# Kernel optimization log

Hardware: AMD Instinct MI355X
Metric: run time of the kernel (lower is better)

The kernel has to match this reference:

```python
import jax, jax.numpy as jnp
import numpy as np

LN_EPS = 1e-5


def _gather(x, idx):
    # x: [B, N, C], idx: [B, N, K] -> [B, N, K, C]
    return jax.vmap(lambda xb, ib: xb[ib])(x, idx)


def setup_inputs() -> dict:
    key = jax.random.key(0)
    ks = jax.random.split(key, 8)
    B, N, K, C_in, C_out, GEO = 2, 16384, 32, 128, 128, 10
    return {
        "points": jax.random.normal(ks[0], (B, N, 3), dtype=jnp.float32),
        "features": jax.random.normal(ks[1], (B, N, C_in), dtype=jnp.float32),
        "grouped_idx": jax.random.randint(ks[2], (B, N, K), 0, N, dtype=jnp.int32),
        "w_pos": jax.random.normal(ks[3], (GEO, C_in), dtype=jnp.float32) * (GEO ** -0.5),
        "b_pos": jnp.zeros((C_in,), jnp.float32),
        "w_gcm": jax.random.normal(ks[4], (C_in, C_in), dtype=jnp.float32) * (C_in ** -0.5),
        "b_gcm": jnp.zeros((C_in,), jnp.float32),
        "w_out": jax.random.normal(ks[5], (C_in, C_out), dtype=jnp.float32) * (C_in ** -0.5),
        "b_out": jnp.zeros((C_out,), jnp.float32),
        "ln_g": jnp.ones((C_out,), jnp.float32),
        "ln_b": jnp.zeros((C_out,), jnp.float32),
    }


def reference(points, features, grouped_idx, w_pos, b_pos, w_gcm, b_gcm,
              w_out, b_out, ln_g, ln_b):
    # gather neighbor coords and features: [B, N, K, *]
    grouped_pts = _gather(points, grouped_idx)
    xyz = points[..., 0:3]                      # [B, N, 3]
    grouped_xyz = grouped_pts[..., 0:3]         # [B, N, K, 3]
    center = xyz[:, :, None, :]                 # [B, N, 1, 3]
    diff = grouped_xyz - center                 # xi - xj
    dist = jnp.linalg.norm(diff, axis=-1, keepdims=True)  # ||xi - xj||
    K = grouped_xyz.shape[2]
    geo = jnp.concatenate(
        [jnp.broadcast_to(center, grouped_xyz.shape), grouped_xyz, diff, dist],
        axis=-1)                                # [B, N, K, 10]
    expanded_f = geo @ w_pos + b_pos            # pos_proj -> [B, N, K, C_in]
    grouped_f = _gather(features, grouped_idx)  # [B, N, K, C_in]
    h = jax.nn.relu((grouped_f + expanded_f) @ w_gcm + b_gcm)  # gcm_layer
    pooled = jnp.max(h, axis=2)                 # maxpooling over neighbors
    res = pooled + features                     # residual
    o = res @ w_out + b_out                     # out Linear
    mu = jnp.mean(o, axis=-1, keepdims=True)
    var = jnp.mean((o - mu) ** 2, axis=-1, keepdims=True)
    o = (o - mu) * jax.lax.rsqrt(var + LN_EPS) * ln_g + ln_b  # LayerNorm
    return jax.nn.relu(o)
```

## Files before the change

kernel.cpp:

```cpp
#include <hip/hip_runtime.h>
#include <hip/hip_bf16.h>
#include <math.h>

typedef __attribute__((ext_vector_type(8))) short short8;
typedef __attribute__((ext_vector_type(4))) float float4v;
typedef unsigned short ushort_t;

constexpr int NPTS = 32768;
constexpr int NN   = 16384;
constexpr int KK   = 32;
constexpr int CC   = 128;
constexpr int GRP  = 16;
constexpr int SG   = 40;
constexpr int SR   = 136;
#define LN_EPS 1e-5f

constexpr size_t WS_WP   = 0;
constexpr size_t WS_WO   = 40960;
constexpr size_t WS_BE   = 73728;
constexpr size_t WS_FB   = 74240;
constexpr size_t WS_NEED = WS_FB + (size_t)NPTS * CC * 2;

__device__ __forceinline__ short f2bs(float x) {
    return (short)__builtin_bit_cast(unsigned short, __float2bfloat16(x));
}
__device__ __forceinline__ float bs2f(ushort_t u) {
    return __uint_as_float(((unsigned)u) << 16);
}

__global__ __launch_bounds__(256) void prep_kernel(
    const float* __restrict__ features,
    const float* __restrict__ w_pos, const float* __restrict__ b_pos,
    const float* __restrict__ w_gcm, const float* __restrict__ b_gcm,
    const float* __restrict__ w_out,
    short* __restrict__ wsWp, short* __restrict__ wsWo, float* __restrict__ wsBeff,
    ushort_t* __restrict__ featbf)
{
    const int t = threadIdx.x;
    const int blk = blockIdx.x;

    if (blk >= 2) {
        const size_t base = (size_t)(blk - 2) * 2048 + (size_t)t * 8;
        const float4* fp = (const float4*)(features + base);
        const float4 a = fp[0], b = fp[1];
        short8 v;
        v[0]=f2bs(a.x); v[1]=f2bs(a.y); v[2]=f2bs(a.z); v[3]=f2bs(a.w);
        v[4]=f2bs(b.x); v[5]=f2bs(b.y); v[6]=f2bs(b.z); v[7]=f2bs(b.w);
        *(short8*)(featbf + base) = v;
        return;
    }
    if (blk == 1) {
        for (int e = t; e < 128 * 128; e += 256) {
            int j = e & 7, n = (e >> 3) & 127, g = e >> 10;
            wsWo[e] = f2bs(w_out[(g * 8 + j) * 128 + n]);
        }
        return;
    }
    __shared__ float sW[128 * 128];
    __shared__ float sPG[10 * 128];
    for (int e = t; e < 4096; e += 256) ((float4*)sW)[e] = ((const float4*)w_gcm)[e];
    __syncthreads();
    {
        const int c  = t & 127;
        const int gb = t >> 7;
        for (int gi = 0; gi < 5; ++gi) {
            const int g = gi * 2 + gb;
            float s = 0.f;
            for (int r = 0; r < 128; ++r) s += w_pos[g * 128 + r] * sW[r * 128 + c];
            sPG[g * 128 + c] = s;
        }
        if (t < 128) {
            float wb = b_gcm[t];
            for (int r = 0; r < 128; ++r) wb += b_pos[r] * sW[r * 128 + t];
            wsBeff[t] = wb;
        }
    }
    __syncthreads();
    for (int e = t; e < 20 * 128 * 8; e += 256) {
        const int j = e & 7, n = (e >> 3) & 127, g = e >> 10;
        const int k = g * 8 + j;
        const float v = (k < 128) ? sW[k * 128 + n] : (k < 138 ? sPG[(k - 128) * 128 + n] : 0.f);
        wsWp[e] = f2bs(v);
    }
}

template<int DMA>
__global__ __launch_bounds__(256) void bridge_main(
    const float* __restrict__ points, const float* __restrict__ features,
    const int*   __restrict__ gidx,
    const short* __restrict__ wsWp, const short* __restrict__ wsWo,
    const float* __restrict__ wsBeff, const ushort_t* __restrict__ featbf,
    const float* __restrict__ b_out, const float* __restrict__ ln_g,
    const float* __restrict__ ln_b,
    float* __restrict__ out)
{
    __shared__ short sA[2][KK * CC];
    __shared__ short sG[2][KK * SG];
    __shared__ short sRes[GRP * SR];
    __shared__ int   sIdx[GRP * KK];
    __shared__ float sPS[4][GRP], sPQ[4][GRP];

    const int t = threadIdx.x, wv = t >> 6, lane = t & 63;
    const int quad = (t >> 4) & 3, m = t & 15;
    const int g0 = blockIdx.x * GRP;
    const int nbase = (g0 >= NN) ? NN : 0;
    const int col0 = wv * 32 + m;

    sIdx[t]       = gidx[(size_t)g0 * KK + t];
    sIdx[t + 256] = gidx[(size_t)g0 * KK + t + 256];
    if (t < 128) {
        const int b = t >> 6, r = (t >> 1) & 31, h = t & 1;
        *(short8*)&sG[b][r * SG + 16 + h * 8] = (short8)0;
    }

    short8 bWp[5][2];
    #pragma unroll
    for (int ks = 0; ks < 5; ++ks)
        #pragma unroll
        for (int ntl = 0; ntl < 2; ++ntl)
            bWp[ks][ntl] = *((const short8*)wsWp + ((ks * 4 + quad) * 128 + col0 + ntl * 16));
    float beffv[2] = { wsBeff[col0], wsBeff[col0 + 16] };

    __syncthreads();

    const int r0 = wv * 4 + (lane >> 4);
    const int pc = lane & 15;
    const int gc = pc ^ r0;

    float4 ff0a, ff0b, ff1a, ff1b;
    float gcx, gcy, gcz, ggx, ggy, ggz;

    auto issue_dma = [&](int p, int buf) {
        const int kn0 = nbase + sIdx[p * KK + r0];
        const int kn1 = nbase + sIdx[p * KK + r0 + 16];
        const ushort_t* gp0 = featbf + (size_t)kn0 * CC + gc * 8;
        const ushort_t* gp1 = featbf + (size_t)kn1 * CC + gc * 8;
        short* l0 = &sA[buf][(wv * 4) * CC];
        short* l1 = &sA[buf][(wv * 4 + 16) * CC];
        __builtin_amdgcn_global_load_lds((const __attribute__((address_space(1))) void*)gp0,
                                         (__attribute__((address_space(3))) void*)l0, 16, 0, 0);
        __builtin_amdgcn_global_load_lds((const __attribute__((address_space(1))) void*)gp1,
                                         (__attribute__((address_space(3))) void*)l1, 16, 0, 0);
    };
    auto fb_load = [&](int p) {
        const int kn0 = nbase + sIdx[p * KK + r0];
        const int kn1 = nbase + sIdx[p * KK + r0 + 16];
        const float4* f0 = (const float4*)(features + (size_t)kn0 * CC + gc * 8);
        const float4* f1 = (const float4*)(features + (size_t)kn1 * CC + gc * 8);
        ff0a = f0[0]; ff0b = f0[1]; ff1a = f1[0]; ff1b = f1[1];
    };
    auto fb_store = [&](int buf) {
        short8 v;
        v[0]=f2bs(ff0a.x); v[1]=f2bs(ff0a.y); v[2]=f2bs(ff0a.z); v[3]=f2bs(ff0a.w);
        v[4]=f2bs(ff0b.x); v[5]=f2bs(ff0b.y); v[6]=f2bs(ff0b.z); v[7]=f2bs(ff0b.w);
        *(short8*)&sA[buf][r0 * CC + pc * 8] = v;
        v[0]=f2bs(ff1a.x); v[1]=f2bs(ff1a.y); v[2]=f2bs(ff1a.z); v[3]=f2bs(ff1a.w);
        v[4]=f2bs(ff1b.x); v[5]=f2bs(ff1b.y); v[6]=f2bs(ff1b.z); v[7]=f2bs(ff1b.w);
        *(short8*)&sA[buf][(r0 + 16) * CC + pc * 8] = v;
    };
    auto geo_load = [&](int p) {
        if (lane < 8) {
            const int j  = wv * 8 + lane;
            const int pt = g0 + p;
            const int kn = nbase + sIdx[p * KK + j];
            gcx = points[(size_t)pt * 3 + 0]; gcy = points[(size_t)pt * 3 + 1]; gcz = points[(size_t)pt * 3 + 2];
            ggx = points[(size_t)kn * 3 + 0]; ggy = points[(size_t)kn * 3 + 1]; ggz = points[(size_t)kn * 3 + 2];
        }
    };
    auto geo_store = [&](int buf) {
        if (lane < 8) {
            const int j = wv * 8 + lane;
            const float dx = ggx - gcx, dy = ggy - gcy, dz = ggz - gcz;
            const float dist = sqrtf(dx * dx + dy * dy + dz * dz);
            short8 v0, v1 = (short8)0;
            v0[0]=f2bs(gcx); v0[1]=f2bs(gcy); v0[2]=f2bs(gcz);
            v0[3]=f2bs(ggx); v0[4]=f2bs(ggy); v0[5]=f2bs(ggz);
            v0[6]=f2bs(dx);  v0[7]=f2bs(dy);
            v1[0]=f2bs(dz);  v1[1]=f2bs(dist);
            *(short8*)&sG[buf][j * SG + 0] = v0;
            *(short8*)&sG[buf][j * SG + 8] = v1;
        }
    };

    if constexpr (DMA) issue_dma(0, 0); else fb_load(0);
    geo_load(0);
    if constexpr (!DMA) fb_store(0);
    geo_store(0);
    __syncthreads();

    int offA[4];
    #pragma unroll
    for (int ks = 0; ks < 4; ++ks) offA[ks] = m * CC + (((ks * 4 + quad) ^ m) * 8);
    const int offG = m * SG + quad * 8;

    for (int p = 0; p < GRP; ++p) {
        const int buf = p & 1, nbuf = buf ^ 1;
        if (p + 1 < GRP) {
            if constexpr (DMA) issue_dma(p + 1, nbuf); else fb_load(p + 1);
            geo_load(p + 1);
        }

        const short* ab = sA[buf];
        const short* ag = sG[buf];
        float4v acc[2][2] = {};
        #pragma unroll
        for (int ks = 0; ks < 4; ++ks) {
            const short8 a0 = *(const short8*)(ab + offA[ks]);
            const short8 a1 = *(const short8*)(ab + offA[ks] + 16 * CC);
            acc[0][0] = __builtin_amdgcn_mfma_f32_16x16x32_bf16(a0, bWp[ks][0], acc[0][0], 0, 0, 0);
            acc[0][1] = __builtin_amdgcn_mfma_f32_16x16x32_bf16(a0, bWp[ks][1], acc[0][1], 0, 0, 0);
            acc[1][0] = __builtin_amdgcn_mfma_f32_16x16x32_bf16(a1, bWp[ks][0], acc[1][0], 0, 0, 0);
            acc[1][1] = __builtin_amdgcn_mfma_f32_16x16x32_bf16(a1, bWp[ks][1], acc[1][1], 0, 0, 0);
        }
        {
            const short8 a0 = *(const short8*)(ag + offG);
            const short8 a1 = *(const short8*)(ag + offG + 16 * SG);
            acc[0][0] = __builtin_amdgcn_mfma_f32_16x16x32_bf16(a0, bWp[4][0], acc[0][0], 0, 0, 0);
            acc[0][1] = __builtin_amdgcn_mfma_f32_16x16x32_bf16(a0, bWp[4][1], acc[0][1], 0, 0, 0);
            acc[1][0] = __builtin_amdgcn_mfma_f32_16x16x32_bf16(a1, bWp[4][0], acc[1][0], 0, 0, 0);
            acc[1][1] = __builtin_amdgcn_mfma_f32_16x16x32_bf16(a1, bWp[4][1], acc[1][1], 0, 0, 0);
        }

        if (p + 1 < GRP) {
            if constexpr (!DMA) fb_store(nbuf);
            geo_store(nbuf);
        }

        const int pt = g0 + p;
        #pragma unroll
        for (int ntl = 0; ntl < 2; ++ntl) {
            float v = acc[0][ntl][0];
            #pragma unroll
            for (int r = 1; r < 4; ++r) v = fmaxf(v, acc[0][ntl][r]);
            #pragma unroll
            for (int r = 0; r < 4; ++r) v = fmaxf(v, acc[1][ntl][r]);
            v = fmaxf(v, __shfl_xor(v, 16));
            v = fmaxf(v, __shfl_xor(v, 32));
            v = fmaxf(v + beffv[ntl], 0.f);
            float fc;
            if constexpr (DMA) fc = bs2f(featbf[(size_t)pt * CC + col0 + ntl * 16]);
            else               fc = features[(size_t)pt * CC + col0 + ntl * 16];
            const float res = v + fc;
            if (quad == 0) sRes[p * SR + col0 + ntl * 16] = f2bs(res);
        }
        __syncthreads();
    }

    short8 bWo[4][2];
    #pragma unroll
    for (int ks = 0; ks < 4; ++ks)
        #pragma unroll
        for (int ntl = 0; ntl < 2; ++ntl)
            bWo[ks][ntl] = *((const short8*)wsWo + ((ks * 4 + quad) * 128 + col0 + ntl * 16));

    const short* rm = sRes + m * SR;
    float4v acc2[2] = {};
    #pragma unroll
    for (int ks = 0; ks < 4; ++ks) {
        const short8 a = *(const short8*)(rm + ks * 32 + quad * 8);
        acc2[0] = __builtin_amdgcn_mfma_f32_16x16x32_bf16(a, bWo[ks][0], acc2[0], 0, 0, 0);
        acc2[1] = __builtin_amdgcn_mfma_f32_16x16x32_bf16(a, bWo[ks][1], acc2[1], 0, 0, 0);
    }

    const float boutv[2] = { b_out[col0], b_out[col0 + 16] };
    const float lngv[2]  = { ln_g[col0], ln_g[col0 + 16] };
    const float lnbv[2]  = { ln_b[col0], ln_b[col0 + 16] };

    #pragma unroll
    for (int r = 0; r < 4; ++r) {
        const float o0 = acc2[0][r] + boutv[0];
        const float o1 = acc2[1][r] + boutv[1];
        float ss = o0 + o1, qq = o0 * o0 + o1 * o1;
        #pragma unroll
        for (int d = 1; d < 16; d <<= 1) { ss += __shfl_xor(ss, d); qq += __shfl_xor(qq, d); }
        if (m == 0) { sPS[wv][quad * 4 + r] = ss; sPQ[wv][quad * 4 + r] = qq; }
    }
    __syncthreads();

    #pragma unroll
    for (int r = 0; r < 4; ++r) {
        const int R = quad * 4 + r;
        const float S = sPS[0][R] + sPS[1][R] + sPS[2][R] + sPS[3][R];
        const float Q = sPQ[0][R] + sPQ[1][R] + sPQ[2][R] + sPQ[3][R];
        const float mu  = S * (1.f / 128.f);
        const float var = fmaxf(Q * (1.f / 128.f) - mu * mu, 0.f);
        const float rstd = rsqrtf(var + LN_EPS);
        const float o0 = acc2[0][r] + boutv[0];
        const float o1 = acc2[1][r] + boutv[1];
        const size_t base = (size_t)(g0 + R) * CC;
        out[base + col0]      = fmaxf((o0 - mu) * rstd * lngv[0] + lnbv[0], 0.f);
        out[base + col0 + 16] = fmaxf((o1 - mu) * rstd * lngv[1] + lnbv[1], 0.f);
    }
}

extern "C" void kernel_launch(void* const* d_in, const int* in_sizes, int n_in,
                              void* d_out, int out_size, void* d_ws, size_t ws_size,
                              hipStream_t stream) {
    const float* points   = (const float*)d_in[0];
    const float* features = (const float*)d_in[1];
    const int*   gidx     = (const int*)  d_in[2];
    const float* w_pos    = (const float*)d_in[3];
    const float* b_pos    = (const float*)d_in[4];
    const float* w_gcm    = (const float*)d_in[5];
    const float* b_gcm    = (const float*)d_in[6];
    const float* w_out    = (const float*)d_in[7];
    const float* b_out    = (const float*)d_in[8];
    const float* ln_g     = (const float*)d_in[9];
    const float* ln_b     = (const float*)d_in[10];
    float* out = (float*)d_out;

    char* ws = (char*)d_ws;
    short*    wsWp   = (short*)(ws + WS_WP);
    short*    wsWo   = (short*)(ws + WS_WO);
    float*    wsBeff = (float*)(ws + WS_BE);
    ushort_t* featbf = (ushort_t*)(ws + WS_FB);

    const bool use_dma = (ws_size >= WS_NEED);
    const int prep_blocks = use_dma ? (2 + NPTS * CC / 2048) : 2;

    hipLaunchKernelGGL(prep_kernel, dim3(prep_blocks), dim3(256), 0, stream,
                       features, w_pos, b_pos, w_gcm, b_gcm, w_out,
                       wsWp, wsWo, wsBeff, featbf);
    if (use_dma) {
        hipLaunchKernelGGL((bridge_main<1>), dim3(NPTS / GRP), dim3(256), 0, stream,
                           points, features, gidx, wsWp, wsWo, wsBeff, featbf,
                           b_out, ln_g, ln_b, out);
    } else {
        hipLaunchKernelGGL((bridge_main<0>), dim3(NPTS / GRP), dim3(256), 0, stream,
                           points, features, gidx, wsWp, wsWo, wsBeff, featbf,
                           b_out, ln_g, ln_b, out);
    }
}
```

Before: 174.9 us.

## Process two points per iteration with waves split by point and channel half

The main loop now handles a pair of points per iteration. Each pair of waves owns one point, and each wave covers 64 output channels (4 column tiles) instead of 32. This halves the loop trips and barriers, doubles the MFMA work per A-fragment load, and prefetches the residual features a stage early. The single prep kernel is split into a two-block weight-prep kernel and a separate feature-conversion kernel, and the w_out transpose is staged through shared memory. In exchange the doubled shared buffers and larger per-thread weight fragments raise register and LDS pressure, which may lower occupancy, and the LayerNorm stores are now done by only half the waves.

```diff
diff --git a/kernel.cpp b/kernel.cpp
--- a/kernel.cpp
+++ b/kernel.cpp
@@ -3,6 +3,7 @@
 #include <math.h>
 
 typedef __attribute__((ext_vector_type(8))) short short8;
+typedef __attribute__((ext_vector_type(4))) short short4v;
 typedef __attribute__((ext_vector_type(4))) float float4v;
 typedef unsigned short ushort_t;
 
@@ -28,36 +29,25 @@
     return __uint_as_float(((unsigned)u) << 16);
 }
 
-__global__ __launch_bounds__(256) void prep_kernel(
-    const float* __restrict__ features,
+__global__ __launch_bounds__(256) void prep_weights(
     const float* __restrict__ w_pos, const float* __restrict__ b_pos,
     const float* __restrict__ w_gcm, const float* __restrict__ b_gcm,
     const float* __restrict__ w_out,
-    short* __restrict__ wsWp, short* __restrict__ wsWo, float* __restrict__ wsBeff,
-    ushort_t* __restrict__ featbf)
+    short* __restrict__ wsWp, short* __restrict__ wsWo, float* __restrict__ wsBeff)
 {
+    __shared__ float sW[128 * 128];
+    __shared__ float sPG[10 * 128];
     const int t = threadIdx.x;
-    const int blk = blockIdx.x;
-
-    if (blk >= 2) {
-        const size_t base = (size_t)(blk - 2) * 2048 + (size_t)t * 8;
-        const float4* fp = (const float4*)(features + base);
-        const float4 a = fp[0], b = fp[1];
-        short8 v;
-        v[0]=f2bs(a.x); v[1]=f2bs(a.y); v[2]=f2bs(a.z); v[3]=f2bs(a.w);
-        v[4]=f2bs(b.x); v[5]=f2bs(b.y); v[6]=f2bs(b.z); v[7]=f2bs(b.w);
-        *(short8*)(featbf + base) = v;
-        return;
-    }
-    if (blk == 1) {
+
+    if (blockIdx.x == 1) {
+        for (int e = t; e < 4096; e += 256) ((float4*)sW)[e] = ((const float4*)w_out)[e];
+        __syncthreads();
         for (int e = t; e < 128 * 128; e += 256) {
             int j = e & 7, n = (e >> 3) & 127, g = e >> 10;
-            wsWo[e] = f2bs(w_out[(g * 8 + j) * 128 + n]);
+            wsWo[e] = f2bs(sW[(g * 8 + j) * 128 + n]);
         }
         return;
     }
-    __shared__ float sW[128 * 128];
-    __shared__ float sPG[10 * 128];
     for (int e = t; e < 4096; e += 256) ((float4*)sW)[e] = ((const float4*)w_gcm)[e];
     __syncthreads();
     {
@@ -81,6 +71,19 @@
         const int k = g * 8 + j;
         const float v = (k < 128) ? sW[k * 128 + n] : (k < 138 ? sPG[(k - 128) * 128 + n] : 0.f);
         wsWp[e] = f2bs(v);
+    }
+}
+
+__global__ __launch_bounds__(256) void prep_convert(
+    const float* __restrict__ features, ushort_t* __restrict__ featbf)
+{
+    const int t = threadIdx.x;
+    #pragma unroll
+    for (int i = 0; i < 8; ++i) {
+        const int f4 = blockIdx.x * 2048 + i * 256 + t;
+        const float4 a = ((const float4*)features)[f4];
+        short4v v; v[0]=f2bs(a.x); v[1]=f2bs(a.y); v[2]=f2bs(a.z); v[3]=f2bs(a.w);
+        ((short4v*)featbf)[f4] = v;
     }
 }
 
@@ -94,82 +97,56 @@
     const float* __restrict__ ln_b,
     float* __restrict__ out)
 {
-    __shared__ short sA[2][KK * CC];
-    __shared__ short sG[2][KK * SG];
+    __shared__ short sA[2][2][KK * CC];
+    __shared__ short sG[2][2][KK * SG];
     __shared__ short sRes[GRP * SR];
     __shared__ int   sIdx[GRP * KK];
     __shared__ float sPS[4][GRP], sPQ[4][GRP];
 
     const int t = threadIdx.x, wv = t >> 6, lane = t & 63;
     const int quad = (t >> 4) & 3, m = t & 15;
+    const int ph = wv >> 1;
+    const int ch = wv & 1;
     const int g0 = blockIdx.x * GRP;
     const int nbase = (g0 >= NN) ? NN : 0;
-    const int col0 = wv * 32 + m;
 
     sIdx[t]       = gidx[(size_t)g0 * KK + t];
     sIdx[t + 256] = gidx[(size_t)g0 * KK + t + 256];
-    if (t < 128) {
-        const int b = t >> 6, r = (t >> 1) & 31, h = t & 1;
-        *(short8*)&sG[b][r * SG + 16 + h * 8] = (short8)0;
-    }
-
-    short8 bWp[5][2];
+    {
+        const int bu = t >> 7, te = (t >> 6) & 1, row = (t >> 1) & 31, h = t & 1;
+        *(short8*)&sG[bu][te][row * SG + 16 + h * 8] = (short8)0;
+    }
+
+    short8 bWp[5][4];
     #pragma unroll
     for (int ks = 0; ks < 5; ++ks)
         #pragma unroll
-        for (int ntl = 0; ntl < 2; ++ntl)
-            bWp[ks][ntl] = *((const short8*)wsWp + ((ks * 4 + quad) * 128 + col0 + ntl * 16));
-    float beffv[2] = { wsBeff[col0], wsBeff[col0 + 16] };
-
-    __syncthreads();
-
-    const int r0 = wv * 4 + (lane >> 4);
-    const int pc = lane & 15;
-    const int gc = pc ^ r0;
-
-    float4 ff0a, ff0b, ff1a, ff1b;
+        for (int n = 0; n < 4; ++n)
+            bWp[ks][n] = *((const short8*)wsWp + ((ks * 4 + quad) * 128 + ch * 64 + n * 16 + m));
+    float beffv[4];
+    #pragma unroll
+    for (int n = 0; n < 4; ++n) beffv[n] = wsBeff[ch * 64 + n * 16 + m];
+
+    __syncthreads();
+
     float gcx, gcy, gcz, ggx, ggy, ggz;
-
-    auto issue_dma = [&](int p, int buf) {
-        const int kn0 = nbase + sIdx[p * KK + r0];
-        const int kn1 = nbase + sIdx[p * KK + r0 + 16];
-        const ushort_t* gp0 = featbf + (size_t)kn0 * CC + gc * 8;
-        const ushort_t* gp1 = featbf + (size_t)kn1 * CC + gc * 8;
-        short* l0 = &sA[buf][(wv * 4) * CC];
-        short* l1 = &sA[buf][(wv * 4 + 16) * CC];
-        __builtin_amdgcn_global_load_lds((const __attribute__((address_space(1))) void*)gp0,
-                                         (__attribute__((address_space(3))) void*)l0, 16, 0, 0);
-        __builtin_amdgcn_global_load_lds((const __attribute__((address_space(1))) void*)gp1,
-                                         (__attribute__((address_space(3))) void*)l1, 16, 0, 0);
-    };
-    auto fb_load = [&](int p) {
-        const int kn0 = nbase + sIdx[p * KK + r0];
-        const int kn1 = nbase + sIdx[p * KK + r0 + 16];
-        const float4* f0 = (const float4*)(features + (size_t)kn0 * CC + gc * 8);
-        const float4* f1 = (const float4*)(features + (size_t)kn1 * CC + gc * 8);
-        ff0a = f0[0]; ff0b = f0[1]; ff1a = f1[0]; ff1b = f1[1];
-    };
-    auto fb_store = [&](int buf) {
-        short8 v;
-        v[0]=f2bs(ff0a.x); v[1]=f2bs(ff0a.y); v[2]=f2bs(ff0a.z); v[3]=f2bs(ff0a.w);
-        v[4]=f2bs(ff0b.x); v[5]=f2bs(ff0b.y); v[6]=f2bs(ff0b.z); v[7]=f2bs(ff0b.w);
-        *(short8*)&sA[buf][r0 * CC + pc * 8] = v;
-        v[0]=f2bs(ff1a.x); v[1]=f2bs(ff1a.y); v[2]=f2bs(ff1a.z); v[3]=f2bs(ff1a.w);
-        v[4]=f2bs(ff1b.x); v[5]=f2bs(ff1b.y); v[6]=f2bs(ff1b.z); v[7]=f2bs(ff1b.w);
-        *(short8*)&sA[buf][(r0 + 16) * CC + pc * 8] = v;
-    };
-    auto geo_load = [&](int p) {
-        if (lane < 8) {
-            const int j  = wv * 8 + lane;
-            const int pt = g0 + p;
-            const int kn = nbase + sIdx[p * KK + j];
+    float resn[4], resc[4];
+    float4 fb0[4], fb1[4];
+
+    auto geo_load = [&](int pair) {
+        if (lane < 16) {
+            const int e = wv * 16 + lane;
+            const int te = e >> 5, row = e & 31;
+            const int pt = g0 + pair * 2 + te;
+            const int kn = nbase + sIdx[(pair * 2 + te) * KK + row];
             gcx = points[(size_t)pt * 3 + 0]; gcy = points[(size_t)pt * 3 + 1]; gcz = points[(size_t)pt * 3 + 2];
             ggx = points[(size_t)kn * 3 + 0]; ggy = points[(size_t)kn * 3 + 1]; ggz = points[(size_t)kn * 3 + 2];
         }
     };
-    auto geo_store = [&](int buf) {
-        if (lane < 8) {
-            const int j = wv * 8 + lane;
+    auto geo_store = [&](int pair, int buf) {
+        if (lane < 16) {
+            const int e = wv * 16 + lane;
+            const int te = e >> 5, row = e & 31;
             const float dx = ggx - gcx, dy = ggy - gcy, dz = ggz - gcz;
             const float dist = sqrtf(dx * dx + dy * dy + dz * dz);
             short8 v0, v1 = (short8)0;
@@ -177,15 +154,57 @@
             v0[3]=f2bs(ggx); v0[4]=f2bs(ggy); v0[5]=f2bs(ggz);
             v0[6]=f2bs(dx);  v0[7]=f2bs(dy);
             v1[0]=f2bs(dz);  v1[1]=f2bs(dist);
-            *(short8*)&sG[buf][j * SG + 0] = v0;
-            *(short8*)&sG[buf][j * SG + 8] = v1;
-        }
-    };
-
-    if constexpr (DMA) issue_dma(0, 0); else fb_load(0);
+            *(short8*)&sG[buf][te][row * SG + 0] = v0;
+            *(short8*)&sG[buf][te][row * SG + 8] = v1;
+        }
+    };
+    auto res_load = [&](int pair) {
+        const int pt = g0 + pair * 2 + ph;
+        #pragma unroll
+        for (int n = 0; n < 4; ++n) {
+            if constexpr (DMA) resn[n] = bs2f(featbf[(size_t)pt * CC + ch * 64 + n * 16 + m]);
+            else               resn[n] = features[(size_t)pt * CC + ch * 64 + n * 16 + m];
+        }
+    };
+    auto gather_issue = [&](int pair, int buf) {
+        #pragma unroll
+        for (int i = 0; i < 4; ++i) {
+            const int e = wv * 4 + i;
+            const int te = e >> 3, rg = e & 7;
+            const int row = rg * 4 + (lane >> 4);
+            const int kn  = nbase + sIdx[(pair * 2 + te) * KK + row];
+            const int gc  = (lane & 15) ^ (row & 15);
+            if constexpr (DMA) {
+                const ushort_t* gp = featbf + (size_t)kn * CC + gc * 8;
+                short* lp = &sA[buf][te][rg * 4 * CC];
+                __builtin_amdgcn_global_load_lds((const __attribute__((address_space(1))) void*)gp,
+                                                 (__attribute__((address_space(3))) void*)lp, 16, 0, 0);
+            } else {
+                const float4* fp = (const float4*)(features + (size_t)kn * CC + gc * 8);
+                fb0[i] = fp[0]; fb1[i] = fp[1];
+            }
+        }
+    };
+    auto gather_store = [&](int buf) {
+        #pragma unroll
+        for (int i = 0; i < 4; ++i) {
+            const int e = wv * 4 + i;
+            const int te = e >> 3, rg = e & 7;
+            const int row = rg * 4 + (lane >> 4);
+            short8 v;
+            v[0]=f2bs(fb0[i].x); v[1]=f2bs(fb0[i].y); v[2]=f2bs(fb0[i].z); v[3]=f2bs(fb0[i].w);
+            v[4]=f2bs(fb1[i].x); v[5]=f2bs(fb1[i].y); v[6]=f2bs(fb1[i].z); v[7]=f2bs(fb1[i].w);
+            *(short8*)&sA[buf][te][row * CC + (lane & 15) * 8] = v;
+        }
+    };
+
     geo_load(0);
-    if constexpr (!DMA) fb_store(0);
-    geo_store(0);
+    res_load(0);
+    gather_issue(0, 0);
+    geo_store(0, 0);
+    if constexpr (!DMA) gather_store(0);
+    #pragma unroll
+    for (int n = 0; n < 4; ++n) resc[n] = resn[n];
     __syncthreads();
 
     int offA[4];
@@ -193,103 +212,115 @@
     for (int ks = 0; ks < 4; ++ks) offA[ks] = m * CC + (((ks * 4 + quad) ^ m) * 8);
     const int offG = m * SG + quad * 8;
 
-    for (int p = 0; p < GRP; ++p) {
-        const int buf = p & 1, nbuf = buf ^ 1;
-        if (p + 1 < GRP) {
-            if constexpr (DMA) issue_dma(p + 1, nbuf); else fb_load(p + 1);
-            geo_load(p + 1);
-        }
-
-        const short* ab = sA[buf];
-        const short* ag = sG[buf];
-        float4v acc[2][2] = {};
+    for (int pair = 0; pair < GRP / 2; ++pair) {
+        const int buf = pair & 1, nb = buf ^ 1;
+        if (pair < GRP / 2 - 1) {
+            geo_load(pair + 1);
+            res_load(pair + 1);
+            gather_issue(pair + 1, nb);
+        }
+
+        const short* at = sA[buf][ph];
+        const short* gt = sG[buf][ph];
+        float4v acc[2][4] = {};
         #pragma unroll
         for (int ks = 0; ks < 4; ++ks) {
-            const short8 a0 = *(const short8*)(ab + offA[ks]);
-            const short8 a1 = *(const short8*)(ab + offA[ks] + 16 * CC);
-            acc[0][0] = __builtin_amdgcn_mfma_f32_16x16x32_bf16(a0, bWp[ks][0], acc[0][0], 0, 0, 0);
-            acc[0][1] = __builtin_amdgcn_mfma_f32_16x16x32_bf16(a0, bWp[ks][1], acc[0][1], 0, 0, 0);
-            acc[1][0] = __builtin_amdgcn_mfma_f32_16x16x32_bf16(a1, bWp[ks][0], acc[1][0], 0, 0, 0);
-            acc[1][1] = __builtin_amdgcn_mfma_f32_16x16x32_bf16(a1, bWp[ks][1], acc[1][1], 0, 0, 0);
+            const short8 a0 = *(const short8*)(at + offA[ks]);
+            const short8 a1 = *(const short8*)(at + offA[ks] + 16 * CC);
+            #pragma unroll
+            for (int n = 0; n < 4; ++n) {
+                acc[0][n] = __builtin_amdgcn_mfma_f32_16x16x32_bf16(a0, bWp[ks][n], acc[0][n], 0, 0, 0);
+                acc[1][n] = __builtin_amdgcn_mfma_f32_16x16x32_bf16(a1, bWp[ks][n], acc[1][n], 0, 0, 0);
+            }
         }
         {
-            const short8 a0 = *(const short8*)(ag + offG);
-            const short8 a1 = *(const short8*)(ag + offG + 16 * SG);
-            acc[0][0] = __builtin_amdgcn_mfma_f32_16x16x32_bf16(a0, bWp[4][0], acc[0][0], 0, 0, 0);
-            acc[0][1] = __builtin_amdgcn_mfma_f32_16x16x32_bf16(a0, bWp[4][1], acc[0][1], 0, 0, 0);
-            acc[1][0] = __builtin_amdgcn_mfma_f32_16x16x32_bf16(a1, bWp[4][0], acc[1][0], 0, 0, 0);
-            acc[1][1] = __builtin_amdgcn_mfma_f32_16x16x32_bf16(a1, bWp[4][1], acc[1][1], 0, 0, 0);
-        }
-
-        if (p + 1 < GRP) {
-            if constexpr (!DMA) fb_store(nbuf);
-            geo_store(nbuf);
-        }
-
-        const int pt = g0 + p;
-        #pragma unroll
-        for (int ntl = 0; ntl < 2; ++ntl) {
-            float v = acc[0][ntl][0];
-            #pragma unroll
-            for (int r = 1; r < 4; ++r) v = fmaxf(v, acc[0][ntl][r]);
-            #pragma unroll
-            for (int r = 0; r < 4; ++r) v = fmaxf(v, acc[1][ntl][r]);
+            const short8 a0 = *(const short8*)(gt + offG);
+            const short8 a1 = *(const short8*)(gt + offG + 16 * SG);
+            #pragma unroll
+            for (int n = 0; n < 4; ++n) {
+                acc[0][n] = __builtin_amdgcn_mfma_f32_16x16x32_bf16(a0, bWp[4][n], acc[0][n], 0, 0, 0);
+                acc[1][n] = __builtin_amdgcn_mfma_f32_16x16x32_bf16(a1, bWp[4][n], acc[1][n], 0, 0, 0);
+            }
+        }
+
+        if (pair < GRP / 2 - 1) {
+            geo_store(pair + 1, nb);
+            if constexpr (!DMA) gather_store(nb);
+        }
+
+        const int prow = pair * 2 + ph;
+        #pragma unroll
+        for (int n = 0; n < 4; ++n) {
+            float v = acc[0][n][0];
+            #pragma unroll
+            for (int r = 1; r < 4; ++r) v = fmaxf(v, acc[0][n][r]);
+            #pragma unroll
+            for (int r = 0; r < 4; ++r) v = fmaxf(v, acc[1][n][r]);
             v = fmaxf(v, __shfl_xor(v, 16));
             v = fmaxf(v, __shfl_xor(v, 32));
-            v = fmaxf(v + beffv[ntl], 0.f);
-            float fc;
-            if constexpr (DMA) fc = bs2f(featbf[(size_t)pt * CC + col0 + ntl * 16]);
-            else               fc = features[(size_t)pt * CC + col0 + ntl * 16];
-            const float res = v + fc;
-            if (quad == 0) sRes[p * SR + col0 + ntl * 16] = f2bs(res);
-        }
+            v = fmaxf(v + beffv[n], 0.f);
+            const float res = v + resc[n];
+            if (quad == 0) sRes[prow * SR + ch * 64 + n * 16 + m] = f2bs(res);
+        }
+        #pragma unroll
+        for (int n = 0; n < 4; ++n) resc[n] = resn[n];
         __syncthreads();
     }
 
-    short8 bWo[4][2];
+    short8 bWo[4][4];
     #pragma unroll
     for (int ks = 0; ks < 4; ++ks)
         #pragma unroll
-        for (int ntl = 0; ntl < 2; ++ntl)
-            bWo[ks][ntl] = *((const short8*)wsWo + ((ks * 4 + quad) * 128 + col0 + ntl * 16));
+        for (int n = 0; n < 4; ++n)
+            bWo[ks][n] = *((const short8*)wsWo + ((ks * 4 + quad) * 128 + ch * 64 + n * 16 + m));
 
     const short* rm = sRes + m * SR;
-    float4v acc2[2] = {};
+    float4v acc2[4] = {};
     #pragma unroll
     for (int ks = 0; ks < 4; ++ks) {
-        const short8 a = *(const short8*)(rm + ks * 32 + quad * 8);
-        acc2[0] = __builtin_amdgcn_mfma_f32_16x16x32_bf16(a, bWo[ks][0], acc2[0], 0, 0, 0);
-        acc2[1] = __builtin_amdgcn_mfma_f32_16x16x32_bf16(a, bWo[ks][1], acc2[1], 0, 0, 0);
-    }
-
-    const float boutv[2] = { b_out[col0], b_out[col0 + 16] };
-    const float lngv[2]  = { ln_g[col0], ln_g[col0 + 16] };
-    const float lnbv[2]  = { ln_b[col0], ln_b[col0 + 16] };
+        const short8 a = *(const short8*)(rm + (ks * 4 + quad) * 8);
+        #pragma unroll
+        for (int n = 0; n < 4; ++n)
+            acc2[n] = __builtin_amdgcn_mfma_f32_16x16x32_bf16(a, bWo[ks][n], acc2[n], 0, 0, 0);
+    }
+
+    float boutv[4], lngv[4], lnbv[4];
+    #pragma unroll
+    for (int n = 0; n < 4; ++n) {
+        const int c = ch * 64 + n * 16 + m;
+        boutv[n] = b_out[c]; lngv[n] = ln_g[c]; lnbv[n] = ln_b[c];
+    }
 
     #pragma unroll
     for (int r = 0; r < 4; ++r) {
-        const float o0 = acc2[0][r] + boutv[0];
-        const float o1 = acc2[1][r] + boutv[1];
-        float ss = o0 + o1, qq = o0 * o0 + o1 * o1;
+        float ss = 0.f, qq = 0.f;
+        #pragma unroll
+        for (int n = 0; n < 4; ++n) {
+            const float o = acc2[n][r] + boutv[n];
+            ss += o; qq += o * o;
+        }
         #pragma unroll
         for (int d = 1; d < 16; d <<= 1) { ss += __shfl_xor(ss, d); qq += __shfl_xor(qq, d); }
         if (m == 0) { sPS[wv][quad * 4 + r] = ss; sPQ[wv][quad * 4 + r] = qq; }
     }
     __syncthreads();
 
-    #pragma unroll
-    for (int r = 0; r < 4; ++r) {
-        const int R = quad * 4 + r;
-        const float S = sPS[0][R] + sPS[1][R] + sPS[2][R] + sPS[3][R];
-        const float Q = sPQ[0][R] + sPQ[1][R] + sPQ[2][R] + sPQ[3][R];
-        const float mu  = S * (1.f / 128.f);
-        const float var = fmaxf(Q * (1.f / 128.f) - mu * mu, 0.f);
-        const float rstd = rsqrtf(var + LN_EPS);
-        const float o0 = acc2[0][r] + boutv[0];
-        const float o1 = acc2[1][r] + boutv[1];
-        const size_t base = (size_t)(g0 + R) * CC;
-        out[base + col0]      = fmaxf((o0 - mu) * rstd * lngv[0] + lnbv[0], 0.f);
-        out[base + col0 + 16] = fmaxf((o1 - mu) * rstd * lngv[1] + lnbv[1], 0.f);
+    if (wv < 2) {
+        #pragma unroll
+        for (int r = 0; r < 4; ++r) {
+            const int R = quad * 4 + r;
+            const float S = (sPS[0][R] + sPS[1][R] + sPS[2][R] + sPS[3][R]) * 0.5f;
+            const float Q = (sPQ[0][R] + sPQ[1][R] + sPQ[2][R] + sPQ[3][R]) * 0.5f;
+            const float mu  = S * (1.f / 128.f);
+            const float var = fmaxf(Q * (1.f / 128.f) - mu * mu, 0.f);
+            const float rstd = rsqrtf(var + LN_EPS);
+            const size_t base = (size_t)(g0 + R) * CC;
+            #pragma unroll
+            for (int n = 0; n < 4; ++n) {
+                const float o = acc2[n][r] + boutv[n];
+                out[base + ch * 64 + n * 16 + m] = fmaxf((o - mu) * rstd * lngv[n] + lnbv[n], 0.f);
+            }
+        }
     }
 }
 
@@ -316,12 +347,11 @@
     ushort_t* featbf = (ushort_t*)(ws + WS_FB);
 
     const bool use_dma = (ws_size >= WS_NEED);
-    const int prep_blocks = use_dma ? (2 + NPTS * CC / 2048) : 2;
-
-    hipLaunchKernelGGL(prep_kernel, dim3(prep_blocks), dim3(256), 0, stream,
-                       features, w_pos, b_pos, w_gcm, b_gcm, w_out,
-                       wsWp, wsWo, wsBeff, featbf);
+
+    hipLaunchKernelGGL(prep_weights, dim3(2), dim3(256), 0, stream,
+                       w_pos, b_pos, w_gcm, b_gcm, w_out, wsWp, wsWo, wsBeff);
     if (use_dma) {
+        hipLaunchKernelGGL(prep_convert, dim3(512), dim3(256), 0, stream, features, featbf);
         hipLaunchKernelGGL((bridge_main<1>), dim3(NPTS / GRP), dim3(256), 0, stream,
                            points, features, gidx, wsWp, wsWo, wsBeff, featbf,
                            b_out, ln_g, ln_b, out);
```

New measurement: 187.8 us. 7.3% more time.
